# Optimization experiments

Measured on AMD Instinct MI355X. Metric: run time of the kernel, lower is better.

The kernel has to match this reference:

```python
import jax, jax.numpy as jnp
import numpy as np

NUM_HEADS = 12
HEAD_DIM = 64
SCALE = HEAD_DIM ** -0.5


def setup_inputs() -> dict:
    key = jax.random.key(0)
    k1, k2, k3, k4, k5 = jax.random.split(key, 5)
    B, N, C = 4, 2048, NUM_HEADS * HEAD_DIM
    x = jax.random.normal(k1, (B, N, C), dtype=jnp.float32)
    W_qkv = jax.random.normal(k2, (C, 3 * C), dtype=jnp.float32) * (C ** -0.5)
    b_qkv = jax.random.normal(k3, (3 * C,), dtype=jnp.float32) * 0.02
    W_proj = jax.random.normal(k4, (C, C), dtype=jnp.float32) * (C ** -0.5)
    b_proj = jax.random.normal(k5, (C,), dtype=jnp.float32) * 0.02
    return {"x": x, "W_qkv": W_qkv, "b_qkv": b_qkv, "W_proj": W_proj, "b_proj": b_proj}


def reference(x, W_qkv, b_qkv, W_proj, b_proj):
    B, N, C = x.shape
    H, D = NUM_HEADS, HEAD_DIM
    qkv = x @ W_qkv + b_qkv                      # [B, N, 3C]
    qkv = qkv.reshape(B, N, 3, H, D)
    q = qkv[:, :, 0].transpose(0, 2, 1, 3) * SCALE  # [B, H, N, D]
    k = qkv[:, :, 1].transpose(0, 2, 1, 3)          # [B, H, N, D]
    v = qkv[:, :, 2].transpose(0, 2, 1, 3)          # [B, H, N, D]
    attn = jnp.einsum("bhnd,bhmd->bhnm", q, k)   # [B, H, N, N]
    attn = jax.nn.softmax(attn, axis=-1)
    ctx = jnp.einsum("bhnm,bhmd->bhnd", attn, v)  # [B, H, N, D]
    attn_out = ctx.transpose(0, 2, 1, 3).reshape(B, N, C)
    out = attn_out @ W_proj + b_proj
    return (out, attn_out)
```

## Files before the change

kernel.cpp:

```cpp
#include <hip/hip_runtime.h>
#include <stdint.h>

typedef unsigned short u16;
using bf16x8 = __attribute__((ext_vector_type(8))) __bf16;
using s16x8  = __attribute__((ext_vector_type(8))) short;
using f32x4  = __attribute__((ext_vector_type(4))) float;

#define SCALE_Q 0.125f
#define LOG2E 1.44269504088896f

__device__ __forceinline__ u16 f2bf(float f) {
  union { float f; uint32_t u; } v; v.f = f;
  uint32_t u = v.u;
  return (u16)((u + 0x7FFFu + ((u >> 16) & 1)) >> 16);
}

__device__ __forceinline__ bf16x8 ld_frag(const u16* p) {
  return __builtin_bit_cast(bf16x8, *(const s16x8*)p);
}

__device__ __forceinline__ f32x4 MF(bf16x8 a, bf16x8 b, f32x4 c) {
  return __builtin_amdgcn_mfma_f32_16x16x32_bf16(a, b, c, 0, 0, 0);
}

__device__ __forceinline__ void gld16(const u16* g, u16* l) {
  __builtin_amdgcn_global_load_lds(
      (const __attribute__((address_space(1))) uint32_t*)g,
      (__attribute__((address_space(3))) uint32_t*)l, 16, 0, 0);
}

__device__ __forceinline__ uint32_t pk_bf16(float a, float b) {
  uint32_t u0 = __builtin_bit_cast(uint32_t, a) + 0x8000u;
  uint32_t u1 = __builtin_bit_cast(uint32_t, b) + 0x8000u;
  return __builtin_amdgcn_perm(u1, u0, 0x07060302u);
}

__global__ void prep_kernel(const float* __restrict__ x, u16* __restrict__ xb,
                            const float* __restrict__ Wq, u16* __restrict__ wqt,
                            const float* __restrict__ Wp, u16* __restrict__ wpt) {
  __shared__ float tile[32][33];
  int bx = blockIdx.x;
  if (bx < 6144) {
    int i = (bx * 256 + threadIdx.x) * 4;
    float4 v = *(const float4*)(x + i);
    uint2 o;
    o.x = (uint32_t)f2bf(v.x) | ((uint32_t)f2bf(v.y) << 16);
    o.y = (uint32_t)f2bf(v.z) | ((uint32_t)f2bf(v.w) << 16);
    *(uint2*)(xb + i) = o;
    return;
  }
  bx -= 6144;
  const float* in;
  u16* out;
  int C, cb, rb;
  const int R = 768;
  if (bx < 1728) { in = Wq; out = wqt; C = 2304; cb = bx % 72; rb = bx / 72; }
  else { bx -= 1728; in = Wp; out = wpt; C = 768; cb = bx % 24; rb = bx / 24; }
  int c0 = cb * 32, r0 = rb * 32;
  int tx = threadIdx.x & 31, ty = threadIdx.x >> 5;
#pragma unroll
  for (int j = 0; j < 32; j += 8)
    tile[ty + j][tx] = in[(size_t)(r0 + ty + j) * C + c0 + tx];
  __syncthreads();
#pragma unroll
  for (int j = 0; j < 32; j += 8)
    out[(size_t)(c0 + ty + j) * R + r0 + tx] = f2bf(tile[tx][ty + j]);
}

__global__ __launch_bounds__(256) void gemm_qkv(
    const u16* __restrict__ A, const u16* __restrict__ Bt, const float* __restrict__ bias,
    u16* __restrict__ q_out, u16* __restrict__ k_out, u16* __restrict__ v_out) {
  constexpr int K = 768;
  __shared__ __align__(16) u16 smem[17408];
  u16* sA = smem;
  u16* sB = smem + 8192;
  const int tid = threadIdx.x;
  const int lane = tid & 63, wave = tid >> 6;
  const int ml = lane & 15, kg = lane >> 4;
  const int wr = wave >> 1, wc = wave & 1;
  const int bn = blockIdx.x, bm = blockIdx.y;

  f32x4 acc[4][4] = {};
  const u16* Abase = A + (size_t)(bm * 128) * K;
  const u16* Bbase = Bt + (size_t)(bn * 128) * K;

  for (int k0 = 0; k0 < K; k0 += 64) {
#pragma unroll
    for (int p = 0; p < 4; p++) {
      int q = p * 256 + tid;
      int r = q >> 3, s = q & 7, c = s ^ (r & 7);
      gld16(Abase + (size_t)r * K + k0 + c * 8, sA + q * 8);
      gld16(Bbase + (size_t)r * K + k0 + c * 8, sB + q * 8);
    }
    __syncthreads();
#pragma unroll
    for (int kc = 0; kc < 2; kc++) {
      bf16x8 af[4], bfr[4];
      int ac = kc * 4 + kg;
#pragma unroll
      for (int i = 0; i < 4; i++) {
        int arow = wr * 64 + i * 16 + ml;
        af[i] = ld_frag(sA + (arow * 8 + (ac ^ (arow & 7))) * 8);
        int brow = wc * 64 + i * 16 + ml;
        bfr[i] = ld_frag(sB + (brow * 8 + (ac ^ (brow & 7))) * 8);
      }
#pragma unroll
      for (int mi = 0; mi < 4; mi++)
#pragma unroll
        for (int ni = 0; ni < 4; ni++)
          acc[mi][ni] = MF(af[mi], bfr[ni], acc[mi][ni]);
    }
    __syncthreads();
  }

  if (bn >= 12) {
    uint32_t* t32 = (uint32_t*)smem;
#pragma unroll
    for (int ni = 0; ni < 4; ni++) {
      int n_local = wc * 64 + ni * 16 + ml;
      float bv = bias[bn * 128 + n_local];
#pragma unroll
      for (int mi = 0; mi < 4; mi++) {
        int mh = wr * 32 + mi * 8 + kg * 2;
        t32[n_local * 68 + mh]     = pk_bf16(acc[mi][ni][0] + bv, acc[mi][ni][1] + bv);
        t32[n_local * 68 + mh + 1] = pk_bf16(acc[mi][ni][2] + bv, acc[mi][ni][3] + bv);
      }
    }
    __syncthreads();
    int row = tid >> 1, seg = tid & 1;
    int dg = (bn - 12) * 128 + row;
    int h = dg >> 6, d = dg & 63;
    int bi = bm >> 4, tok0 = (bm & 15) * 128;
    u16* dst = v_out + ((size_t)(bi * 12 + h) * 64 + d) * 2048 + tok0 + seg * 64;
    const uint32_t* src = t32 + row * 68 + seg * 32;
#pragma unroll
    for (int j = 0; j < 8; j++)
      *(uint4*)(dst + j * 8) = *(const uint4*)(src + j * 4);
  } else {
    u16* dst = (bn < 6) ? q_out : k_out;
    float scl = (bn < 6) ? SCALE_Q * LOG2E : 1.0f;
#pragma unroll
    for (int ni = 0; ni < 4; ni++) {
      int n = bn * 128 + wc * 64 + ni * 16 + ml;
      int rem = (bn < 6) ? n : n - 768;
      int h = rem >> 6, d = rem & 63;
      float bv = bias[n];
#pragma unroll
      for (int mi = 0; mi < 4; mi++) {
        int m0 = bm * 128 + wr * 64 + mi * 16 + kg * 4;
#pragma unroll
        for (int r = 0; r < 4; r++) {
          int m = m0 + r;
          int bi = m >> 11, tok = m & 2047;
          dst[(size_t)(bi * 12 + h) * 131072 + (size_t)tok * 64 + d] = f2bf((acc[mi][ni][r] + bv) * scl);
        }
      }
    }
  }
}

__global__ __launch_bounds__(256) void gemm_proj(
    const u16* __restrict__ A, const u16* __restrict__ Bt, const float* __restrict__ bias,
    float* __restrict__ c_out) {
  constexpr int K = 768;
  __shared__ __align__(16) u16 sA[128 * 64];
  __shared__ __align__(16) u16 sB[64 * 64];
  const int tid = threadIdx.x;
  const int lane = tid & 63, wave = tid >> 6;
  const int ml = lane & 15, kg = lane >> 4;
  const int bn = blockIdx.x, bm = blockIdx.y;
  f32x4 acc[2][4] = {};
  const u16* Abase = A + (size_t)(bm * 128) * K;
  const u16* Bbase = Bt + (size_t)(bn * 64) * K;

  for (int k0 = 0; k0 < K; k0 += 64) {
#pragma unroll
    for (int p = 0; p < 4; p++) {
      int q = p * 256 + tid;
      int r = q >> 3, s = q & 7, c = s ^ (r & 7);
      gld16(Abase + (size_t)r * K + k0 + c * 8, sA + q * 8);
    }
#pragma unroll
    for (int p = 0; p < 2; p++) {
      int q = p * 256 + tid;
      int r = q >> 3, s = q & 7, c = s ^ (r & 7);
      gld16(Bbase + (size_t)r * K + k0 + c * 8, sB + q * 8);
    }
    __syncthreads();
#pragma unroll
    for (int kc = 0; kc < 2; kc++) {
      int ac = kc * 4 + kg;
      bf16x8 af[2], bfr[4];
#pragma unroll
      for (int i = 0; i < 2; i++) {
        int arow = wave * 32 + i * 16 + ml;
        af[i] = ld_frag(sA + (arow * 8 + (ac ^ (arow & 7))) * 8);
      }
#pragma unroll
      for (int i = 0; i < 4; i++) {
        int brow = i * 16 + ml;
        bfr[i] = ld_frag(sB + (brow * 8 + (ac ^ (brow & 7))) * 8);
      }
#pragma unroll
      for (int mi = 0; mi < 2; mi++)
#pragma unroll
        for (int ni = 0; ni < 4; ni++)
          acc[mi][ni] = MF(af[mi], bfr[ni], acc[mi][ni]);
    }
    __syncthreads();
  }
#pragma unroll
  for (int ni = 0; ni < 4; ni++) {
    int n = bn * 64 + ni * 16 + ml;
    float bv = bias[n];
#pragma unroll
    for (int mi = 0; mi < 2; mi++) {
      int m0 = bm * 128 + wave * 32 + mi * 16 + kg * 4;
#pragma unroll
      for (int r = 0; r < 4; r++)
        c_out[(size_t)(m0 + r) * 768 + n] = acc[mi][ni][r] + bv;
    }
  }
}

__global__ __launch_bounds__(256, 3) void attn_kernel(
    const u16* __restrict__ qs, const u16* __restrict__ ks, const u16* __restrict__ vt,
    float* __restrict__ attn_f32, u16* __restrict__ attn_bf) {
  __shared__ __align__(16) u16 sK[2][4096];
  __shared__ __align__(16) u16 sV[2][4096];
  __shared__ __align__(16) u16 sP[4][2304];
  const int tid = threadIdx.x, lane = tid & 63, wave = tid >> 6;
  const int ml = lane & 15, kg = lane >> 4;
  const int bid  = blockIdx.x + (blockIdx.y << 4);
  const int slot = bid >> 3;
  const int bh   = (bid & 7) * 6 + (slot >> 4);
  const int q0   = (slot & 15) * 128 + wave * 32;
  const size_t base = (size_t)bh * 131072;

  bf16x8 qf[2][2];
#pragma unroll
  for (int qt = 0; qt < 2; qt++) {
    const u16* qp = qs + base + (size_t)(q0 + qt * 16 + ml) * 64 + kg * 8;
    qf[qt][0] = ld_frag(qp);
    qf[qt][1] = ld_frag(qp + 32);
  }
  f32x4 l4[2] = {};
  f32x4 O[2][4] = {};

  const int m7 = ml & 7;
  const u16* kbase[2] = { &sK[0][ml * 64 + ((0 + kg) ^ m7) * 8],
                          &sK[0][ml * 64 + ((4 + kg) ^ m7) * 8] };
  const u16* vbase[2] = { &sV[0][ml * 64 + ((0 + kg) ^ m7) * 8],
                          &sV[0][ml * 64 + ((4 + kg) ^ m7) * 8] };
  u16* pw = &sP[wave][ml * 72 + kg * 4];
  const u16* pr = &sP[wave][ml * 72 + kg * 8];

  const int r0 = tid >> 3,          c0 = (tid & 7) ^ (r0 & 7);
  const int r1 = (256 + tid) >> 3,  c1 = (tid & 7) ^ (r1 & 7);
  const u16* kgp0 = ks + base + r0 * 64 + c0 * 8;
  const u16* kgp1 = ks + base + r1 * 64 + c1 * 8;
  const u16* vgp0 = vt + base + r0 * 2048 + c0 * 8;
  const u16* vgp1 = vt + base + r1 * 2048 + c1 * 8;

  auto stage = [&](int b, int kt) {
    gld16(kgp0 + kt * 64, &sK[b][tid * 8]);
    gld16(kgp1 + kt * 64, &sK[b][2048 + tid * 8]);
    gld16(vgp0 + kt,      &sV[b][tid * 8]);
    gld16(vgp1 + kt,      &sV[b][2048 + tid * 8]);
  };

  stage(0, 0);
  for (int kt = 0; kt < 2048; kt += 128) {
#pragma unroll
    for (int half = 0; half < 2; half++) {
      const int cur = kt + half * 64;
      __syncthreads();
      if (cur + 64 < 2048) stage(half ^ 1, cur + 64);

      f32x4 sc[2][4] = {};
#pragma unroll
      for (int nt = 0; nt < 4; nt++)
#pragma unroll
        for (int kc = 0; kc < 2; kc++) {
          bf16x8 kf = ld_frag(kbase[kc] + nt * 1024 + half * 4096);
          sc[0][nt] = MF(kf, qf[0][kc], sc[0][nt]);
          sc[1][nt] = MF(kf, qf[1][kc], sc[1][nt]);
        }

#pragma unroll
      for (int qt = 0; qt < 2; qt++)
#pragma unroll
        for (int nt = 0; nt < 4; nt++) {
          f32x4 p;
#pragma unroll
          for (int r = 0; r < 4; r++) p[r] = __builtin_amdgcn_exp2f(sc[qt][nt][r]);
          l4[qt] += p;
          uint2 w;
          w.x = pk_bf16(p[0], p[1]);
          w.y = pk_bf16(p[2], p[3]);
          *(uint2*)(pw + qt * 1152 + nt * 16) = w;
        }

      asm volatile("s_waitcnt lgkmcnt(0)" ::: "memory");

#pragma unroll
      for (int kc = 0; kc < 2; kc++) {
        bf16x8 pf0 = ld_frag(pr + kc * 32);
        bf16x8 pf1 = ld_frag(pr + 1152 + kc * 32);
#pragma unroll
        for (int nt2 = 0; nt2 < 4; nt2++) {
          bf16x8 vf = ld_frag(vbase[kc] + nt2 * 1024 + half * 4096);
          O[0][nt2] = MF(pf0, vf, O[0][nt2]);
          O[1][nt2] = MF(pf1, vf, O[1][nt2]);
        }
      }
    }
  }

  float linv[2];
#pragma unroll
  for (int qt = 0; qt < 2; qt++) {
    float s = l4[qt][0] + l4[qt][1] + l4[qt][2] + l4[qt][3];
    s += __shfl_xor(s, 16);
    s += __shfl_xor(s, 32);
    linv[qt] = __builtin_amdgcn_rcpf(s);
  }
  int b = bh / 12, h = bh - b * 12;
#pragma unroll
  for (int qt = 0; qt < 2; qt++)
#pragma unroll
    for (int r = 0; r < 4; r++) {
      float inv = __shfl(linv[qt], kg * 4 + r, 64);
      int qrow = q0 + qt * 16 + kg * 4 + r;
      size_t rowoff = ((size_t)(b * 2048 + qrow)) * 768 + h * 64;
#pragma unroll
      for (int nt2 = 0; nt2 < 4; nt2++) {
        float v = O[qt][nt2][r] * inv;
        int d = nt2 * 16 + ml;
        attn_f32[rowoff + d] = v;
        attn_bf[rowoff + d] = f2bf(v);
      }
    }
}

extern "C" void kernel_launch(void* const* d_in, const int* in_sizes, int n_in,
                              void* d_out, int out_size, void* d_ws, size_t ws_size,
                              hipStream_t stream) {
  const float* x      = (const float*)d_in[0];
  const float* W_qkv  = (const float*)d_in[1];
  const float* b_qkv  = (const float*)d_in[2];
  const float* W_proj = (const float*)d_in[3];
  const float* b_proj = (const float*)d_in[4];
  float* out      = (float*)d_out;
  float* attn_out = out + (size_t)8192 * 768;

  char* ws = (char*)d_ws;
  const size_t SZ_XB = (size_t)8192 * 768 * 2;
  u16* xb      = (u16*)(ws);
  u16* wqkv_t  = (u16*)(ws + SZ_XB);
  u16* wproj_t = (u16*)(ws + SZ_XB + 3538944);
  u16* qs      = (u16*)(ws + SZ_XB + 3538944 + 1179648);
  u16* ks      = (u16*)((char*)qs + SZ_XB);
  u16* vt      = (u16*)((char*)ks + SZ_XB);
  u16* ab      = xb;

  prep_kernel<<<6144 + 1728 + 576, 256, 0, stream>>>(x, xb, W_qkv, wqkv_t, W_proj, wproj_t);
  gemm_qkv<<<dim3(18, 64), 256, 0, stream>>>(xb, wqkv_t, b_qkv, qs, ks, vt);
  attn_kernel<<<dim3(16, 48), 256, 0, stream>>>(qs, ks, vt, attn_out, ab);
  gemm_proj<<<dim3(12, 64), 256, 0, stream>>>(ab, wproj_t, b_proj, out);
}
```

Baseline: 224.3 us.

## Swizzle GEMM block order and interleave softmax exp with PV MFMAs in attention

Both GEMM kernels remap linear block IDs so that consecutive blocks are spread across groups of eight, which changes which tiles run concurrently and aims at better L2/XCD locality. The attention inner loop splits the exp/pack work for the two query tiles so the exp of the second tile can overlap with the PV MFMAs of the first. It also wraps the MFMA sections in s_setprio to favour matrix-issuing waves. V fragments are now kept in registers for reuse, which raises register pressure and may lower occupancy.

```diff
diff --git a/kernel.cpp b/kernel.cpp
--- a/kernel.cpp
+++ b/kernel.cpp
@@ -78,7 +78,9 @@
   const int lane = tid & 63, wave = tid >> 6;
   const int ml = lane & 15, kg = lane >> 4;
   const int wr = wave >> 1, wc = wave & 1;
-  const int bn = blockIdx.x, bm = blockIdx.y;
+  const int bid0 = blockIdx.x + blockIdx.y * 18;
+  const int nbid = (bid0 & 7) * 144 + (bid0 >> 3);
+  const int bn = nbid % 18, bm = nbid / 18;
 
   f32x4 acc[4][4] = {};
   const u16* Abase = A + (size_t)(bm * 128) * K;
@@ -168,7 +170,9 @@
   const int tid = threadIdx.x;
   const int lane = tid & 63, wave = tid >> 6;
   const int ml = lane & 15, kg = lane >> 4;
-  const int bn = blockIdx.x, bm = blockIdx.y;
+  const int bid0 = blockIdx.x + blockIdx.y * 12;
+  const int nbid = (bid0 & 7) * 96 + (bid0 >> 3);
+  const int bn = nbid % 12, bm = nbid / 12;
   f32x4 acc[2][4] = {};
   const u16* Abase = A + (size_t)(bm * 128) * K;
   const u16* Bbase = Bt + (size_t)(bn * 64) * K;
@@ -278,6 +282,7 @@
       if (cur + 64 < 2048) stage(half ^ 1, cur + 64);
 
       f32x4 sc[2][4] = {};
+      __builtin_amdgcn_s_setprio(1);
 #pragma unroll
       for (int nt = 0; nt < 4; nt++)
 #pragma unroll
@@ -286,34 +291,56 @@
           sc[0][nt] = MF(kf, qf[0][kc], sc[0][nt]);
           sc[1][nt] = MF(kf, qf[1][kc], sc[1][nt]);
         }
-
-#pragma unroll
-      for (int qt = 0; qt < 2; qt++)
-#pragma unroll
-        for (int nt = 0; nt < 4; nt++) {
-          f32x4 p;
-#pragma unroll
-          for (int r = 0; r < 4; r++) p[r] = __builtin_amdgcn_exp2f(sc[qt][nt][r]);
-          l4[qt] += p;
-          uint2 w;
-          w.x = pk_bf16(p[0], p[1]);
-          w.y = pk_bf16(p[2], p[3]);
-          *(uint2*)(pw + qt * 1152 + nt * 16) = w;
-        }
-
+      __builtin_amdgcn_s_setprio(0);
+
+#pragma unroll
+      for (int nt = 0; nt < 4; nt++) {
+        f32x4 p;
+#pragma unroll
+        for (int r = 0; r < 4; r++) p[r] = __builtin_amdgcn_exp2f(sc[0][nt][r]);
+        l4[0] += p;
+        uint2 w;
+        w.x = pk_bf16(p[0], p[1]);
+        w.y = pk_bf16(p[2], p[3]);
+        *(uint2*)(pw + nt * 16) = w;
+      }
       asm volatile("s_waitcnt lgkmcnt(0)" ::: "memory");
 
+      bf16x8 vf[2][4];
+      __builtin_amdgcn_s_setprio(1);
 #pragma unroll
       for (int kc = 0; kc < 2; kc++) {
         bf16x8 pf0 = ld_frag(pr + kc * 32);
+#pragma unroll
+        for (int nt2 = 0; nt2 < 4; nt2++) {
+          vf[kc][nt2] = ld_frag(vbase[kc] + nt2 * 1024 + half * 4096);
+          O[0][nt2] = MF(pf0, vf[kc][nt2], O[0][nt2]);
+        }
+      }
+      __builtin_amdgcn_s_setprio(0);
+
+#pragma unroll
+      for (int nt = 0; nt < 4; nt++) {
+        f32x4 p;
+#pragma unroll
+        for (int r = 0; r < 4; r++) p[r] = __builtin_amdgcn_exp2f(sc[1][nt][r]);
+        l4[1] += p;
+        uint2 w;
+        w.x = pk_bf16(p[0], p[1]);
+        w.y = pk_bf16(p[2], p[3]);
+        *(uint2*)(pw + 1152 + nt * 16) = w;
+      }
+      asm volatile("s_waitcnt lgkmcnt(0)" ::: "memory");
+
+      __builtin_amdgcn_s_setprio(1);
+#pragma unroll
+      for (int kc = 0; kc < 2; kc++) {
         bf16x8 pf1 = ld_frag(pr + 1152 + kc * 32);
 #pragma unroll
-        for (int nt2 = 0; nt2 < 4; nt2++) {
-          bf16x8 vf = ld_frag(vbase[kc] + nt2 * 1024 + half * 4096);
-          O[0][nt2] = MF(pf0, vf, O[0][nt2]);
-          O[1][nt2] = MF(pf1, vf, O[1][nt2]);
-        }
-      }
+        for (int nt2 = 0; nt2 < 4; nt2++)
+          O[1][nt2] = MF(pf1, vf[kc][nt2], O[1][nt2]);
+      }
+      __builtin_amdgcn_s_setprio(0);
     }
   }
 
```

Result: no change. 223.3 us (-0.4%).

## Keep softmax probabilities in registers and halve attention query tile per block

Applied to the files above, without the earlier changes.

The attention kernel now gives each wave 16 query rows instead of 32, and each block 64 rows instead of 128, so the grid doubles and occupancy is raised to 4 blocks. The P matrix no longer round-trips through shared memory: the S accumulator layout is reused directly as the A operand of the PV MFMA, and V fragments are gathered with split 8-byte loads to match. Both GEMMs also remap block IDs so consecutive blocks are spread across XCD-sized groups. Smaller query tiles mean K/V tiles are loaded from global memory twice as often per query row, in exchange for less LDS traffic, no extra wait, and more parallelism.

```diff
diff --git a/kernel.cpp b/kernel.cpp
--- a/kernel.cpp
+++ b/kernel.cpp
@@ -78,7 +78,9 @@
   const int lane = tid & 63, wave = tid >> 6;
   const int ml = lane & 15, kg = lane >> 4;
   const int wr = wave >> 1, wc = wave & 1;
-  const int bn = blockIdx.x, bm = blockIdx.y;
+  const int bid0 = blockIdx.x + blockIdx.y * 18;
+  const int nbid = (bid0 & 7) * 144 + (bid0 >> 3);
+  const int bn = nbid % 18, bm = nbid / 18;
 
   f32x4 acc[4][4] = {};
   const u16* Abase = A + (size_t)(bm * 128) * K;
@@ -168,7 +170,9 @@
   const int tid = threadIdx.x;
   const int lane = tid & 63, wave = tid >> 6;
   const int ml = lane & 15, kg = lane >> 4;
-  const int bn = blockIdx.x, bm = blockIdx.y;
+  const int bid0 = blockIdx.x + blockIdx.y * 12;
+  const int nbid = (bid0 & 7) * 96 + (bid0 >> 3);
+  const int bn = nbid % 12, bm = nbid / 12;
   f32x4 acc[2][4] = {};
   const u16* Abase = A + (size_t)(bm * 128) * K;
   const u16* Bbase = Bt + (size_t)(bn * 64) * K;
@@ -223,37 +227,36 @@
   }
 }
 
-__global__ __launch_bounds__(256, 3) void attn_kernel(
+__global__ __launch_bounds__(256, 4) void attn_kernel(
     const u16* __restrict__ qs, const u16* __restrict__ ks, const u16* __restrict__ vt,
     float* __restrict__ attn_f32, u16* __restrict__ attn_bf) {
   __shared__ __align__(16) u16 sK[2][4096];
   __shared__ __align__(16) u16 sV[2][4096];
-  __shared__ __align__(16) u16 sP[4][2304];
   const int tid = threadIdx.x, lane = tid & 63, wave = tid >> 6;
   const int ml = lane & 15, kg = lane >> 4;
-  const int bid  = blockIdx.x + (blockIdx.y << 4);
+  const int m7 = ml & 7;
+  const int bid  = blockIdx.x + (blockIdx.y << 5);
   const int slot = bid >> 3;
-  const int bh   = (bid & 7) * 6 + (slot >> 4);
-  const int q0   = (slot & 15) * 128 + wave * 32;
+  const int bh   = (bid & 7) * 6 + (slot >> 5);
+  const int q0   = (slot & 31) * 64 + wave * 16;
   const size_t base = (size_t)bh * 131072;
 
-  bf16x8 qf[2][2];
-#pragma unroll
-  for (int qt = 0; qt < 2; qt++) {
-    const u16* qp = qs + base + (size_t)(q0 + qt * 16 + ml) * 64 + kg * 8;
-    qf[qt][0] = ld_frag(qp);
-    qf[qt][1] = ld_frag(qp + 32);
-  }
-  f32x4 l4[2] = {};
-  f32x4 O[2][4] = {};
-
-  const int m7 = ml & 7;
+  bf16x8 qf[2];
+  {
+    const u16* qp = qs + base + (size_t)(q0 + ml) * 64 + kg * 8;
+    qf[0] = ld_frag(qp);
+    qf[1] = ld_frag(qp + 32);
+  }
+  f32x4 l4 = {};
+  f32x4 O[4] = {};
+
   const u16* kbase[2] = { &sK[0][ml * 64 + ((0 + kg) ^ m7) * 8],
                           &sK[0][ml * 64 + ((4 + kg) ^ m7) * 8] };
-  const u16* vbase[2] = { &sV[0][ml * 64 + ((0 + kg) ^ m7) * 8],
-                          &sV[0][ml * 64 + ((4 + kg) ^ m7) * 8] };
-  u16* pw = &sP[wave][ml * 72 + kg * 4];
-  const u16* pr = &sP[wave][ml * 72 + kg * 8];
+  const u16* vp[4] = {
+    &sV[0][ml * 64 + ((0 + (kg >> 1)) ^ m7) * 8 + 4 * (kg & 1)],
+    &sV[0][ml * 64 + ((2 + (kg >> 1)) ^ m7) * 8 + 4 * (kg & 1)],
+    &sV[0][ml * 64 + ((4 + (kg >> 1)) ^ m7) * 8 + 4 * (kg & 1)],
+    &sV[0][ml * 64 + ((6 + (kg >> 1)) ^ m7) * 8 + 4 * (kg & 1)] };
 
   const int r0 = tid >> 3,          c0 = (tid & 7) ^ (r0 & 7);
   const int r1 = (256 + tid) >> 3,  c1 = (tid & 7) ^ (r1 & 7);
@@ -277,70 +280,63 @@
       __syncthreads();
       if (cur + 64 < 2048) stage(half ^ 1, cur + 64);
 
-      f32x4 sc[2][4] = {};
+      f32x4 sc[4] = {};
 #pragma unroll
       for (int nt = 0; nt < 4; nt++)
 #pragma unroll
         for (int kc = 0; kc < 2; kc++) {
           bf16x8 kf = ld_frag(kbase[kc] + nt * 1024 + half * 4096);
-          sc[0][nt] = MF(kf, qf[0][kc], sc[0][nt]);
-          sc[1][nt] = MF(kf, qf[1][kc], sc[1][nt]);
+          sc[nt] = MF(kf, qf[kc], sc[nt]);
         }
 
-#pragma unroll
-      for (int qt = 0; qt < 2; qt++)
-#pragma unroll
-        for (int nt = 0; nt < 4; nt++) {
-          f32x4 p;
-#pragma unroll
-          for (int r = 0; r < 4; r++) p[r] = __builtin_amdgcn_exp2f(sc[qt][nt][r]);
-          l4[qt] += p;
-          uint2 w;
-          w.x = pk_bf16(p[0], p[1]);
-          w.y = pk_bf16(p[2], p[3]);
-          *(uint2*)(pw + qt * 1152 + nt * 16) = w;
+      uint32_t w[4][2];
+#pragma unroll
+      for (int nt = 0; nt < 4; nt++) {
+        f32x4 p;
+#pragma unroll
+        for (int r = 0; r < 4; r++) p[r] = __builtin_amdgcn_exp2f(sc[nt][r]);
+        l4 += p;
+        w[nt][0] = pk_bf16(p[0], p[1]);
+        w[nt][1] = pk_bf16(p[2], p[3]);
+      }
+      uint4 u0; u0.x = w[0][0]; u0.y = w[0][1]; u0.z = w[1][0]; u0.w = w[1][1];
+      uint4 u1; u1.x = w[2][0]; u1.y = w[2][1]; u1.z = w[3][0]; u1.w = w[3][1];
+      bf16x8 pf0 = __builtin_bit_cast(bf16x8, u0);
+      bf16x8 pf1 = __builtin_bit_cast(bf16x8, u1);
+
+#pragma unroll
+      for (int c = 0; c < 2; c++) {
+        bf16x8 pf = c ? pf1 : pf0;
+#pragma unroll
+        for (int nt2 = 0; nt2 < 4; nt2++) {
+          uint2 lo = *(const uint2*)(vp[2 * c]     + nt2 * 1024 + half * 4096);
+          uint2 hi = *(const uint2*)(vp[2 * c + 1] + nt2 * 1024 + half * 4096);
+          uint4 uv; uv.x = lo.x; uv.y = lo.y; uv.z = hi.x; uv.w = hi.y;
+          bf16x8 vf = __builtin_bit_cast(bf16x8, uv);
+          O[nt2] = MF(pf, vf, O[nt2]);
         }
-
-      asm volatile("s_waitcnt lgkmcnt(0)" ::: "memory");
-
-#pragma unroll
-      for (int kc = 0; kc < 2; kc++) {
-        bf16x8 pf0 = ld_frag(pr + kc * 32);
-        bf16x8 pf1 = ld_frag(pr + 1152 + kc * 32);
-#pragma unroll
-        for (int nt2 = 0; nt2 < 4; nt2++) {
-          bf16x8 vf = ld_frag(vbase[kc] + nt2 * 1024 + half * 4096);
-          O[0][nt2] = MF(pf0, vf, O[0][nt2]);
-          O[1][nt2] = MF(pf1, vf, O[1][nt2]);
-        }
-      }
-    }
-  }
-
-  float linv[2];
-#pragma unroll
-  for (int qt = 0; qt < 2; qt++) {
-    float s = l4[qt][0] + l4[qt][1] + l4[qt][2] + l4[qt][3];
-    s += __shfl_xor(s, 16);
-    s += __shfl_xor(s, 32);
-    linv[qt] = __builtin_amdgcn_rcpf(s);
-  }
+      }
+    }
+  }
+
+  float s = l4[0] + l4[1] + l4[2] + l4[3];
+  s += __shfl_xor(s, 16);
+  s += __shfl_xor(s, 32);
+  float linv = __builtin_amdgcn_rcpf(s);
   int b = bh / 12, h = bh - b * 12;
 #pragma unroll
-  for (int qt = 0; qt < 2; qt++)
-#pragma unroll
-    for (int r = 0; r < 4; r++) {
-      float inv = __shfl(linv[qt], kg * 4 + r, 64);
-      int qrow = q0 + qt * 16 + kg * 4 + r;
-      size_t rowoff = ((size_t)(b * 2048 + qrow)) * 768 + h * 64;
-#pragma unroll
-      for (int nt2 = 0; nt2 < 4; nt2++) {
-        float v = O[qt][nt2][r] * inv;
-        int d = nt2 * 16 + ml;
-        attn_f32[rowoff + d] = v;
-        attn_bf[rowoff + d] = f2bf(v);
-      }
-    }
+  for (int r = 0; r < 4; r++) {
+    float inv = __shfl(linv, kg * 4 + r, 64);
+    int qrow = q0 + kg * 4 + r;
+    size_t rowoff = ((size_t)(b * 2048 + qrow)) * 768 + h * 64;
+#pragma unroll
+    for (int nt2 = 0; nt2 < 4; nt2++) {
+      float v = O[nt2][r] * inv;
+      int d = nt2 * 16 + ml;
+      attn_f32[rowoff + d] = v;
+      attn_bf[rowoff + d] = f2bf(v);
+    }
+  }
 }
 
 extern "C" void kernel_launch(void* const* d_in, const int* in_sizes, int n_in,
@@ -366,6 +362,6 @@
 
   prep_kernel<<<6144 + 1728 + 576, 256, 0, stream>>>(x, xb, W_qkv, wqkv_t, W_proj, wproj_t);
   gemm_qkv<<<dim3(18, 64), 256, 0, stream>>>(xb, wqkv_t, b_qkv, qs, ks, vt);
-  attn_kernel<<<dim3(16, 48), 256, 0, stream>>>(qs, ks, vt, attn_out, ab);
+  attn_kernel<<<dim3(32, 48), 256, 0, stream>>>(qs, ks, vt, attn_out, ab);
   gemm_proj<<<dim3(12, 64), 256, 0, stream>>>(ab, wproj_t, b_proj, out);
 }
```

After: 236.1 us. +5.3%, slower.

## Keep softmax probabilities in registers and permute V layout; swizzle GEMM block order

Applied to the files above, without the earlier changes.

The attention kernel no longer round-trips the exponentiated scores through per-wave shared memory. It packs them directly into MFMA operand registers, relying on a permuted token order inside the V tile that the QKV GEMM epilogue now writes out. This removes LDS writes, reads and a wait per tile, and frees shared memory that could raise occupancy. Both GEMMs also remap block indices so that consecutive blocks are interleaved, aiming at better cache locality. The trade-off is a fragile coupling between the V store permutation and the register fragment layout.

```diff
diff --git a/kernel.cpp b/kernel.cpp
--- a/kernel.cpp
+++ b/kernel.cpp
@@ -78,7 +78,9 @@
   const int lane = tid & 63, wave = tid >> 6;
   const int ml = lane & 15, kg = lane >> 4;
   const int wr = wave >> 1, wc = wave & 1;
-  const int bn = blockIdx.x, bm = blockIdx.y;
+  const int bid0 = blockIdx.x + blockIdx.y * 18;
+  const int nbid = (bid0 & 7) * 144 + (bid0 >> 3);
+  const int bn = nbid % 18, bm = nbid / 18;
 
   f32x4 acc[4][4] = {};
   const u16* Abase = A + (size_t)(bm * 128) * K;
@@ -132,10 +134,15 @@
     int h = dg >> 6, d = dg & 63;
     int bi = bm >> 4, tok0 = (bm & 15) * 128;
     u16* dst = v_out + ((size_t)(bi * 12 + h) * 64 + d) * 2048 + tok0 + seg * 64;
-    const uint32_t* src = t32 + row * 68 + seg * 32;
-#pragma unroll
-    for (int j = 0; j < 8; j++)
-      *(uint4*)(dst + j * 8) = *(const uint4*)(src + j * 4);
+    const uint32_t* srow = t32 + row * 68;
+#pragma unroll
+    for (int j = 0; j < 8; j++) {
+      int m8 = seg * 8 + j;
+      int c = m8 >> 2, k = m8 & 3;
+      const uint32_t* s = srow + 16 * c + 2 * k;
+      uint4 u; u.x = s[0]; u.y = s[1]; u.z = s[8]; u.w = s[9];
+      *(uint4*)(dst + j * 8) = u;
+    }
   } else {
     u16* dst = (bn < 6) ? q_out : k_out;
     float scl = (bn < 6) ? SCALE_Q * LOG2E : 1.0f;
@@ -168,7 +175,9 @@
   const int tid = threadIdx.x;
   const int lane = tid & 63, wave = tid >> 6;
   const int ml = lane & 15, kg = lane >> 4;
-  const int bn = blockIdx.x, bm = blockIdx.y;
+  const int bid0 = blockIdx.x + blockIdx.y * 12;
+  const int nbid = (bid0 & 7) * 96 + (bid0 >> 3);
+  const int bn = nbid % 12, bm = nbid / 12;
   f32x4 acc[2][4] = {};
   const u16* Abase = A + (size_t)(bm * 128) * K;
   const u16* Bbase = Bt + (size_t)(bn * 64) * K;
@@ -228,9 +237,9 @@
     float* __restrict__ attn_f32, u16* __restrict__ attn_bf) {
   __shared__ __align__(16) u16 sK[2][4096];
   __shared__ __align__(16) u16 sV[2][4096];
-  __shared__ __align__(16) u16 sP[4][2304];
   const int tid = threadIdx.x, lane = tid & 63, wave = tid >> 6;
   const int ml = lane & 15, kg = lane >> 4;
+  const int m7 = ml & 7;
   const int bid  = blockIdx.x + (blockIdx.y << 4);
   const int slot = bid >> 3;
   const int bh   = (bid & 7) * 6 + (slot >> 4);
@@ -247,13 +256,10 @@
   f32x4 l4[2] = {};
   f32x4 O[2][4] = {};
 
-  const int m7 = ml & 7;
   const u16* kbase[2] = { &sK[0][ml * 64 + ((0 + kg) ^ m7) * 8],
                           &sK[0][ml * 64 + ((4 + kg) ^ m7) * 8] };
   const u16* vbase[2] = { &sV[0][ml * 64 + ((0 + kg) ^ m7) * 8],
                           &sV[0][ml * 64 + ((4 + kg) ^ m7) * 8] };
-  u16* pw = &sP[wave][ml * 72 + kg * 4];
-  const u16* pr = &sP[wave][ml * 72 + kg * 8];
 
   const int r0 = tid >> 3,          c0 = (tid & 7) ^ (r0 & 7);
   const int r1 = (256 + tid) >> 3,  c1 = (tid & 7) ^ (r1 & 7);
@@ -287,33 +293,35 @@
           sc[1][nt] = MF(kf, qf[1][kc], sc[1][nt]);
         }
 
+      bf16x8 pf[2][2];
 #pragma unroll
       for (int qt = 0; qt < 2; qt++)
 #pragma unroll
-        for (int nt = 0; nt < 4; nt++) {
-          f32x4 p;
-#pragma unroll
-          for (int r = 0; r < 4; r++) p[r] = __builtin_amdgcn_exp2f(sc[qt][nt][r]);
-          l4[qt] += p;
-          uint2 w;
-          w.x = pk_bf16(p[0], p[1]);
-          w.y = pk_bf16(p[2], p[3]);
-          *(uint2*)(pw + qt * 1152 + nt * 16) = w;
+        for (int c = 0; c < 2; c++) {
+          f32x4 pa, pb;
+#pragma unroll
+          for (int r = 0; r < 4; r++) {
+            pa[r] = __builtin_amdgcn_exp2f(sc[qt][2 * c][r]);
+            pb[r] = __builtin_amdgcn_exp2f(sc[qt][2 * c + 1][r]);
+          }
+          l4[qt] += pa;
+          l4[qt] += pb;
+          uint4 u;
+          u.x = pk_bf16(pa[0], pa[1]);
+          u.y = pk_bf16(pa[2], pa[3]);
+          u.z = pk_bf16(pb[0], pb[1]);
+          u.w = pk_bf16(pb[2], pb[3]);
+          pf[qt][c] = __builtin_bit_cast(bf16x8, u);
         }
 
-      asm volatile("s_waitcnt lgkmcnt(0)" ::: "memory");
-
-#pragma unroll
-      for (int kc = 0; kc < 2; kc++) {
-        bf16x8 pf0 = ld_frag(pr + kc * 32);
-        bf16x8 pf1 = ld_frag(pr + 1152 + kc * 32);
+#pragma unroll
+      for (int c = 0; c < 2; c++)
 #pragma unroll
         for (int nt2 = 0; nt2 < 4; nt2++) {
-          bf16x8 vf = ld_frag(vbase[kc] + nt2 * 1024 + half * 4096);
-          O[0][nt2] = MF(pf0, vf, O[0][nt2]);
-          O[1][nt2] = MF(pf1, vf, O[1][nt2]);
+          bf16x8 vf = ld_frag(vbase[c] + nt2 * 1024 + half * 4096);
+          O[0][nt2] = MF(pf[0][c], vf, O[0][nt2]);
+          O[1][nt2] = MF(pf[1][c], vf, O[1][nt2]);
         }
-      }
     }
   }
 
```

New measurement: 213.8 us. -4.7%, faster.
